# Optimization experiments

Measured on AMD Instinct MI355X. Metric: run time of the kernel, lower is better.

The kernel has to match this reference:

```python
import jax, jax.numpy as jnp
import numpy as np

D_MODEL = 1024
NUM_HEADS = 16
HEAD_DIM = D_MODEL // NUM_HEADS


def setup_inputs() -> dict:
    key = jax.random.key(0)
    ks = jax.random.split(key, 11)
    B, S = 4, 2048
    s = 1.0 / np.sqrt(D_MODEL)
    inp = {
        'query': jax.random.normal(ks[0], (B, S, D_MODEL), jnp.float32),
        'key': jax.random.normal(ks[1], (B, S, D_MODEL), jnp.float32),
        'value': jax.random.normal(ks[2], (B, S, D_MODEL), jnp.float32),
        'W_q': jax.random.normal(ks[3], (D_MODEL, D_MODEL), jnp.float32) * s,
        'b_q': jnp.zeros((D_MODEL,), jnp.float32),
        'W_k': jax.random.normal(ks[4], (D_MODEL, D_MODEL), jnp.float32) * s,
        'b_k': jnp.zeros((D_MODEL,), jnp.float32),
        'W_v': jax.random.normal(ks[5], (D_MODEL, D_MODEL), jnp.float32) * s,
        'b_v': jnp.zeros((D_MODEL,), jnp.float32),
        'W_o': jax.random.normal(ks[6], (D_MODEL, D_MODEL), jnp.float32) * s,
        'b_o': jnp.zeros((D_MODEL,), jnp.float32),
    }
    return inp


def reference(query, key, value, W_q, b_q, W_k, b_k, W_v, b_v, W_o, b_o):
    B, S, _ = query.shape
    # Linear projections (torch Linear: x @ W.T + b)
    Q = query @ W_q.T + b_q
    K = key @ W_k.T + b_k
    V = value @ W_v.T + b_v
    # [B, H, S, Dh]
    def split_heads(x):
        return x.reshape(B, -1, NUM_HEADS, HEAD_DIM).transpose(0, 2, 1, 3)
    Qh, Kh, Vh = split_heads(Q), split_heads(K), split_heads(V)
    scale = 1.0 / jnp.sqrt(jnp.float32(HEAD_DIM))
    scores = jnp.einsum('bhqd,bhkd->bhqk', Qh, Kh) * scale
    attn = jax.nn.softmax(scores, axis=-1)
    out = jnp.einsum('bhqk,bhkd->bhqd', attn, Vh)
    out = out.transpose(0, 2, 1, 3).reshape(B, S, D_MODEL)
    return out @ W_o.T + b_o
```

## Files before the change

kernel.cpp:

```cpp
#include <hip/hip_runtime.h>


#define BATCH 4
#define SEQ   2048
#define NH    16
#define DH    64
#define DM    1024
#define LOG2E 1.4426950408889634f
#define CSC   (0.125f * LOG2E)

typedef __attribute__((ext_vector_type(8))) short s16x8;
typedef __attribute__((ext_vector_type(4))) float f32x4;
typedef const __attribute__((address_space(1))) unsigned int* gas1;
typedef __attribute__((address_space(3))) unsigned int* las3;

__device__ __forceinline__ unsigned short f2bf(float f) {
  unsigned int u = __float_as_uint(f);
  u += 0x7FFFu + ((u >> 16) & 1u);
  return (unsigned short)(u >> 16);
}

__device__ __forceinline__ unsigned int cvt_pk_bf16(float lo, float hi) {
  unsigned int r;
  asm("v_cvt_pk_bf16_f32 %0, %1, %2" : "=v"(r) : "v"(lo), "v"(hi));
  return r;
}

__global__ __launch_bounds__(256) void cvt_bf16_k(const float* __restrict__ in,
                                                  unsigned short* __restrict__ out, int n4) {
  int i = blockIdx.x * 256 + threadIdx.x;
  if (i < n4) {
    float4 v = ((const float4*)in)[i];
    ushort4 o;
    o.x = f2bf(v.x); o.y = f2bf(v.y); o.z = f2bf(v.z); o.w = f2bf(v.w);
    ((ushort4*)out)[i] = o;
  }
}

template<bool BIAS_ROW, bool OUT_F32>
__global__ __launch_bounds__(256) void gemm_bt(const unsigned short* __restrict__ A,
                                               const unsigned short* __restrict__ Bm,
                                               const float* __restrict__ bias,
                                               void* __restrict__ Cout,
                                               int M, int N, int K) {
  __shared__ unsigned short As[128 * 64];
  __shared__ unsigned short Bs[128 * 64];
  const int tid = threadIdx.x;
  const int wave = tid >> 6, lane = tid & 63;
  const int lr = lane & 15, lh = lane >> 4;
  const int tM = blockIdx.y, tN = blockIdx.x;
  const int wm = (wave >> 1) * 64, wn = (wave & 1) * 64;
  f32x4 acc[4][4] = {};

  for (int k0 = 0; k0 < K; k0 += 64) {
    __syncthreads();
#pragma unroll
    for (int i = 0; i < 4; ++i) {
      const int slot = wave * 256 + i * 64 + lane;
      const int row = slot >> 3;
      const int cg = (slot & 7) ^ (row & 7);
      const unsigned short* ga = A  + (size_t)(tM * 128 + row) * K + k0 + cg * 8;
      const unsigned short* gb = Bm + (size_t)(tN * 128 + row) * K + k0 + cg * 8;
      __builtin_amdgcn_global_load_lds((gas1)ga, (las3)(As + (wave * 256 + i * 64) * 8), 16, 0, 0);
      __builtin_amdgcn_global_load_lds((gas1)gb, (las3)(Bs + (wave * 256 + i * 64) * 8), 16, 0, 0);
    }
    __syncthreads();

    s16x8 af[4][2], bfr[4][2];
#pragma unroll
    for (int mt = 0; mt < 4; ++mt) {
#pragma unroll
      for (int kt = 0; kt < 2; ++kt) {
        const int ra = wm + mt * 16 + lr;
        af[mt][kt] = *(const s16x8*)(As + ra * 64 + (((kt * 4 + lh) ^ (ra & 7)) * 8));
        const int rb = wn + mt * 16 + lr;
        bfr[mt][kt] = *(const s16x8*)(Bs + rb * 64 + (((kt * 4 + lh) ^ (rb & 7)) * 8));
      }
    }
#pragma unroll
    for (int mt = 0; mt < 4; ++mt) {
#pragma unroll
      for (int nt = 0; nt < 4; ++nt) {
        acc[mt][nt] = __builtin_amdgcn_mfma_f32_16x16x32_bf16(af[mt][0], bfr[nt][0], acc[mt][nt], 0, 0, 0);
        acc[mt][nt] = __builtin_amdgcn_mfma_f32_16x16x32_bf16(af[mt][1], bfr[nt][1], acc[mt][nt], 0, 0, 0);
      }
    }
  }

#pragma unroll
  for (int mt = 0; mt < 4; ++mt) {
#pragma unroll
    for (int nt = 0; nt < 4; ++nt) {
      const int row0 = tM * 128 + wm + mt * 16 + lh * 4;
      const int col  = tN * 128 + wn + nt * 16 + lr;
      const float bc = BIAS_ROW ? 0.f : bias[col];
#pragma unroll
      for (int r = 0; r < 4; ++r) {
        const float v = acc[mt][nt][r] + (BIAS_ROW ? bias[row0 + r] : bc);
        if (OUT_F32) ((float*)Cout)[(size_t)(row0 + r) * N + col] = v;
        else ((unsigned short*)Cout)[(size_t)(row0 + r) * N + col] = f2bf(v);
      }
    }
  }
}

__global__ __launch_bounds__(256) void attn_k(const unsigned short* __restrict__ Q,
                                              const unsigned short* __restrict__ Kp,
                                              const unsigned short* __restrict__ Vt,
                                              unsigned short* __restrict__ AO) {
  __shared__ unsigned short Ks[64 * 64];
  __shared__ unsigned short Vs[64 * 64];
  __shared__ unsigned short Ps[4 * 32 * 64];
  const int tid = threadIdx.x;
  const int w = tid >> 6, lane = tid & 63;
  const int lr = lane & 15, lh = lane >> 4;
  const int sw = lr & 7;

  const int id = blockIdx.x;
  const int g  = (id & 7) * 128 + (id >> 3);
  const int qt = g & 15;
  const int hb = g >> 4;
  const int h = hb & 15, b = hb >> 4;

  s16x8 qf[2][2];
#pragma unroll
  for (int qb = 0; qb < 2; ++qb)
#pragma unroll
    for (int kt = 0; kt < 2; ++kt)
      qf[qb][kt] = *(const s16x8*)(Q + (size_t)(b * SEQ + qt * 128 + w * 32 + qb * 16 + lr) * DM
                                     + h * DH + kt * 32 + lh * 8);

  f32x4 o[2][4] = {};
  float m_run[2] = {-1e30f, -1e30f};
  float l_run[2] = {0.f, 0.f};
  unsigned short* Pw = Ps + w * 2048;

  for (int kv0 = 0; kv0 < SEQ; kv0 += 64) {
    __syncthreads();
#pragma unroll
    for (int i = 0; i < 2; ++i) {
      const int slot = i * 256 + w * 64 + lane;
      const int row = slot >> 3;
      const int cg = (slot & 7) ^ (row & 7);
      const unsigned short* gk = Kp + (size_t)(b * SEQ + kv0 + row) * DM + h * DH + cg * 8;
      const unsigned short* gv = Vt + (size_t)(h * DH + row) * (BATCH * SEQ) + b * SEQ + kv0 + cg * 8;
      __builtin_amdgcn_global_load_lds((gas1)gk, (las3)(Ks + (i * 256 + w * 64) * 8), 16, 0, 0);
      __builtin_amdgcn_global_load_lds((gas1)gv, (las3)(Vs + (i * 256 + w * 64) * 8), 16, 0, 0);
    }
    __syncthreads();

    f32x4 s[2][4] = {};
#pragma unroll
    for (int nt = 0; nt < 4; ++nt) {
#pragma unroll
      for (int kt = 0; kt < 2; ++kt) {
        const s16x8 kf = *(const s16x8*)(Ks + (nt * 16 + lr) * 64 + (((kt * 4 + lh) ^ sw) * 8));
        s[0][nt] = __builtin_amdgcn_mfma_f32_16x16x32_bf16(kf, qf[0][kt], s[0][nt], 0, 0, 0);
        s[1][nt] = __builtin_amdgcn_mfma_f32_16x16x32_bf16(kf, qf[1][kt], s[1][nt], 0, 0, 0);
      }
    }

#pragma unroll
    for (int qb = 0; qb < 2; ++qb) {
      float mx = fmaxf(fmaxf(s[qb][0][0], s[qb][0][1]), fmaxf(s[qb][0][2], s[qb][0][3]));
#pragma unroll
      for (int nt = 1; nt < 4; ++nt)
        mx = fmaxf(mx, fmaxf(fmaxf(s[qb][nt][0], s[qb][nt][1]),
                             fmaxf(s[qb][nt][2], s[qb][nt][3])));
      mx = fmaxf(mx, __shfl_xor(mx, 16));
      mx = fmaxf(mx, __shfl_xor(mx, 32));
      if (!__all(mx - m_run[qb] <= 64.0f)) {
        const float al = __builtin_amdgcn_exp2f((m_run[qb] - mx) * CSC);
        m_run[qb] = mx;
        l_run[qb] *= al;
#pragma unroll
        for (int dt = 0; dt < 4; ++dt) o[qb][dt] *= al;
      }
      const float base = m_run[qb] * CSC;
      float p[4][4];
      float rs = 0.f;
#pragma unroll
      for (int nt = 0; nt < 4; ++nt)
#pragma unroll
        for (int r = 0; r < 4; ++r) {
          p[nt][r] = __builtin_amdgcn_exp2f(s[qb][nt][r] * CSC - base);
          rs += p[nt][r];
        }
      rs += __shfl_xor(rs, 16);
      rs += __shfl_xor(rs, 32);
      l_run[qb] += rs;

      const int qrow = qb * 16 + lr;
#pragma unroll
      for (int nt = 0; nt < 4; ++nt) {
        uint2 wd;
        wd.x = cvt_pk_bf16(p[nt][0], p[nt][1]);
        wd.y = cvt_pk_bf16(p[nt][2], p[nt][3]);
        const int c8 = nt * 2 + (lh >> 1);
        *(uint2*)(Pw + qrow * 64 + (((c8 ^ sw) << 3) | ((lh & 1) << 2))) = wd;
      }
    }

#pragma unroll
    for (int nb = 0; nb < 2; ++nb) {
      const s16x8 pf0 = *(const s16x8*)(Pw + lr * 64        + (((nb * 4 + lh) ^ sw) * 8));
      const s16x8 pf1 = *(const s16x8*)(Pw + (16 + lr) * 64 + (((nb * 4 + lh) ^ sw) * 8));
#pragma unroll
      for (int dt = 0; dt < 4; ++dt) {
        const s16x8 vf = *(const s16x8*)(Vs + (dt * 16 + lr) * 64 + (((nb * 4 + lh) ^ sw) * 8));
        o[0][dt] = __builtin_amdgcn_mfma_f32_16x16x32_bf16(vf, pf0, o[0][dt], 0, 0, 0);
        o[1][dt] = __builtin_amdgcn_mfma_f32_16x16x32_bf16(vf, pf1, o[1][dt], 0, 0, 0);
      }
    }
  }

#pragma unroll
  for (int qb = 0; qb < 2; ++qb) {
    const float rl = __builtin_amdgcn_rcpf(l_run[qb]);
    unsigned short* orow = AO + (size_t)(b * SEQ + qt * 128 + w * 32 + qb * 16 + lr) * DM + h * DH;
#pragma unroll
    for (int dt = 0; dt < 4; ++dt) {
      *(unsigned int*)(orow + dt * 16 + lh * 4)     = cvt_pk_bf16(o[qb][dt][0] * rl, o[qb][dt][1] * rl);
      *(unsigned int*)(orow + dt * 16 + lh * 4 + 2) = cvt_pk_bf16(o[qb][dt][2] * rl, o[qb][dt][3] * rl);
    }
  }
}

extern "C" void kernel_launch(void* const* d_in, const int* in_sizes, int n_in,
                              void* d_out, int out_size, void* d_ws, size_t ws_size,
                              hipStream_t stream) {
  const float* q   = (const float*)d_in[0];
  const float* k   = (const float*)d_in[1];
  const float* v   = (const float*)d_in[2];
  const float* W_q = (const float*)d_in[3];
  const float* b_q = (const float*)d_in[4];
  const float* W_k = (const float*)d_in[5];
  const float* b_k = (const float*)d_in[6];
  const float* W_v = (const float*)d_in[7];
  const float* b_v = (const float*)d_in[8];
  const float* W_o = (const float*)d_in[9];
  const float* b_o = (const float*)d_in[10];

  const size_t SD  = (size_t)BATCH * SEQ * DM;
  const size_t SDB = SD * 2;
  const size_t D2  = (size_t)DM * DM;
  if (ws_size < 5 * SDB + D2 * 2) return;

  char* base = (char*)d_ws;
  unsigned short* B0 = (unsigned short*)(base);
  unsigned short* B1 = (unsigned short*)(base + 1 * SDB);
  unsigned short* B2 = (unsigned short*)(base + 2 * SDB);
  unsigned short* B3 = (unsigned short*)(base + 3 * SDB);
  unsigned short* B4 = (unsigned short*)(base + 4 * SDB);
  unsigned short* Wb = (unsigned short*)(base + 5 * SDB);

  const int nSD4 = (int)(SD / 4), nD24 = (int)(D2 / 4);
  const dim3 blk(256);
  const dim3 gP(DM / 128, (BATCH * SEQ) / 128);
  const dim3 gV((BATCH * SEQ) / 128, DM / 128);
  const dim3 gA(16 * NH * BATCH);

  cvt_bf16_k<<<nSD4 / 256, blk, 0, stream>>>(q, B0, nSD4);
  cvt_bf16_k<<<nD24 / 256, blk, 0, stream>>>(W_q, Wb, nD24);
  gemm_bt<false, false><<<gP, blk, 0, stream>>>(B0, Wb, b_q, B3, BATCH * SEQ, DM, DM);
  cvt_bf16_k<<<nSD4 / 256, blk, 0, stream>>>(k, B1, nSD4);
  cvt_bf16_k<<<nD24 / 256, blk, 0, stream>>>(W_k, Wb, nD24);
  gemm_bt<false, false><<<gP, blk, 0, stream>>>(B1, Wb, b_k, B4, BATCH * SEQ, DM, DM);
  cvt_bf16_k<<<nSD4 / 256, blk, 0, stream>>>(v, B2, nSD4);
  cvt_bf16_k<<<nD24 / 256, blk, 0, stream>>>(W_v, Wb, nD24);
  gemm_bt<true, false><<<gV, blk, 0, stream>>>(Wb, B2, b_v, B1, DM, BATCH * SEQ, DM);
  attn_k<<<gA, blk, 0, stream>>>(B3, B4, B1, B0);
  cvt_bf16_k<<<nD24 / 256, blk, 0, stream>>>(W_o, Wb, nD24);
  gemm_bt<false, true><<<gP, blk, 0, stream>>>(B0, Wb, b_o, d_out, BATCH * SEQ, DM, DM);
}
```

Baseline: 255.0 us.

## Batch conversions and Q/K projections into fewer launches, double-buffer attention K/V

Merges the three activation conversions and the four weight conversions into two batched launches, and runs the Q and K projections together in one grid along z. Converted weights are staged in the output buffer until the final GEMM overwrites it. The attention kernel gains double-buffered K/V shared memory with explicit vmcnt waits, so the next tile loads while the current one computes. The goal is less launch overhead, better GPU fill, and hidden load latency, at the cost of twice the LDS use in attention, which may reduce occupancy.

Result: faster. 244.4 us (-4.1%).

```diff
diff --git a/kernel.cpp b/kernel.cpp
--- a/kernel.cpp
+++ b/kernel.cpp
@@ -26,29 +26,52 @@
   return r;
 }
 
-__global__ __launch_bounds__(256) void cvt_bf16_k(const float* __restrict__ in,
-                                                  unsigned short* __restrict__ out, int n4) {
+__global__ __launch_bounds__(256) void cvt3_k(const float* __restrict__ s0,
+                                              const float* __restrict__ s1,
+                                              const float* __restrict__ s2,
+                                              unsigned short* __restrict__ d0,
+                                              unsigned short* __restrict__ d1,
+                                              unsigned short* __restrict__ d2, int n4) {
+  const float* s = blockIdx.y == 0 ? s0 : blockIdx.y == 1 ? s1 : s2;
+  unsigned short* d = blockIdx.y == 0 ? d0 : blockIdx.y == 1 ? d1 : d2;
   int i = blockIdx.x * 256 + threadIdx.x;
   if (i < n4) {
-    float4 v = ((const float4*)in)[i];
+    float4 v = ((const float4*)s)[i];
     ushort4 o;
     o.x = f2bf(v.x); o.y = f2bf(v.y); o.z = f2bf(v.z); o.w = f2bf(v.w);
-    ((ushort4*)out)[i] = o;
+    ((ushort4*)d)[i] = o;
+  }
+}
+
+__global__ __launch_bounds__(256) void cvt4_k(const float* __restrict__ s0,
+                                              const float* __restrict__ s1,
+                                              const float* __restrict__ s2,
+                                              const float* __restrict__ s3,
+                                              unsigned short* __restrict__ d0,
+                                              unsigned short* __restrict__ d1,
+                                              unsigned short* __restrict__ d2,
+                                              unsigned short* __restrict__ d3, int n4) {
+  const float* s = blockIdx.y == 0 ? s0 : blockIdx.y == 1 ? s1 : blockIdx.y == 2 ? s2 : s3;
+  unsigned short* d = blockIdx.y == 0 ? d0 : blockIdx.y == 1 ? d1 : blockIdx.y == 2 ? d2 : d3;
+  int i = blockIdx.x * 256 + threadIdx.x;
+  if (i < n4) {
+    float4 v = ((const float4*)s)[i];
+    ushort4 o;
+    o.x = f2bf(v.x); o.y = f2bf(v.y); o.z = f2bf(v.z); o.w = f2bf(v.w);
+    ((ushort4*)d)[i] = o;
   }
 }
 
 template<bool BIAS_ROW, bool OUT_F32>
-__global__ __launch_bounds__(256) void gemm_bt(const unsigned short* __restrict__ A,
-                                               const unsigned short* __restrict__ Bm,
-                                               const float* __restrict__ bias,
-                                               void* __restrict__ Cout,
-                                               int M, int N, int K) {
-  __shared__ unsigned short As[128 * 64];
-  __shared__ unsigned short Bs[128 * 64];
+__device__ __forceinline__ void gemm_core(const unsigned short* __restrict__ A,
+                                          const unsigned short* __restrict__ Bm,
+                                          const float* __restrict__ bias,
+                                          void* __restrict__ Cout,
+                                          int M, int N, int K, int tM, int tN,
+                                          unsigned short* As, unsigned short* Bs) {
   const int tid = threadIdx.x;
   const int wave = tid >> 6, lane = tid & 63;
   const int lr = lane & 15, lh = lane >> 4;
-  const int tM = blockIdx.y, tN = blockIdx.x;
   const int wm = (wave >> 1) * 64, wn = (wave & 1) * 64;
   f32x4 acc[4][4] = {};
 
@@ -104,12 +127,38 @@
   }
 }
 
+template<bool BIAS_ROW, bool OUT_F32>
+__global__ __launch_bounds__(256) void gemm_bt(const unsigned short* __restrict__ A,
+                                               const unsigned short* __restrict__ Bm,
+                                               const float* __restrict__ bias,
+                                               void* __restrict__ Cout, int M, int N, int K) {
+  __shared__ unsigned short As[128 * 64];
+  __shared__ unsigned short Bs[128 * 64];
+  gemm_core<BIAS_ROW, OUT_F32>(A, Bm, bias, Cout, M, N, K, blockIdx.y, blockIdx.x, As, Bs);
+}
+
+__global__ __launch_bounds__(256) void gemm_qk(const unsigned short* __restrict__ A0,
+                                               const unsigned short* __restrict__ A1,
+                                               const unsigned short* __restrict__ W0,
+                                               const unsigned short* __restrict__ W1,
+                                               const float* __restrict__ c0,
+                                               const float* __restrict__ c1,
+                                               void* __restrict__ C0, void* __restrict__ C1,
+                                               int M, int N, int K) {
+  __shared__ unsigned short As[128 * 64];
+  __shared__ unsigned short Bs[128 * 64];
+  if (blockIdx.z == 0)
+    gemm_core<false, false>(A0, W0, c0, C0, M, N, K, blockIdx.y, blockIdx.x, As, Bs);
+  else
+    gemm_core<false, false>(A1, W1, c1, C1, M, N, K, blockIdx.y, blockIdx.x, As, Bs);
+}
+
 __global__ __launch_bounds__(256) void attn_k(const unsigned short* __restrict__ Q,
                                               const unsigned short* __restrict__ Kp,
                                               const unsigned short* __restrict__ Vt,
                                               unsigned short* __restrict__ AO) {
-  __shared__ unsigned short Ks[64 * 64];
-  __shared__ unsigned short Vs[64 * 64];
+  __shared__ unsigned short Ks[2][64 * 64];
+  __shared__ unsigned short Vs[2][64 * 64];
   __shared__ unsigned short Ps[4 * 32 * 64];
   const int tid = threadIdx.x;
   const int w = tid >> 6, lane = tid & 63;
@@ -129,32 +178,50 @@
     for (int kt = 0; kt < 2; ++kt)
       qf[qb][kt] = *(const s16x8*)(Q + (size_t)(b * SEQ + qt * 128 + w * 32 + qb * 16 + lr) * DM
                                      + h * DH + kt * 32 + lh * 8);
+  asm volatile("s_waitcnt vmcnt(0)" ::: "memory");
+  __builtin_amdgcn_sched_barrier(0);
 
   f32x4 o[2][4] = {};
   float m_run[2] = {-1e30f, -1e30f};
   float l_run[2] = {0.f, 0.f};
   unsigned short* Pw = Ps + w * 2048;
 
-  for (int kv0 = 0; kv0 < SEQ; kv0 += 64) {
-    __syncthreads();
+  const unsigned short* Kbase = Kp + (size_t)b * SEQ * DM + h * DH;
+  const unsigned short* Vbase = Vt + (size_t)h * DH * (BATCH * SEQ) + (size_t)b * SEQ;
+
+  auto stage = [&](int buf, int kv0) {
 #pragma unroll
     for (int i = 0; i < 2; ++i) {
       const int slot = i * 256 + w * 64 + lane;
       const int row = slot >> 3;
       const int cg = (slot & 7) ^ (row & 7);
-      const unsigned short* gk = Kp + (size_t)(b * SEQ + kv0 + row) * DM + h * DH + cg * 8;
-      const unsigned short* gv = Vt + (size_t)(h * DH + row) * (BATCH * SEQ) + b * SEQ + kv0 + cg * 8;
-      __builtin_amdgcn_global_load_lds((gas1)gk, (las3)(Ks + (i * 256 + w * 64) * 8), 16, 0, 0);
-      __builtin_amdgcn_global_load_lds((gas1)gv, (las3)(Vs + (i * 256 + w * 64) * 8), 16, 0, 0);
-    }
-    __syncthreads();
+      const unsigned short* gk = Kbase + (size_t)(kv0 + row) * DM + cg * 8;
+      const unsigned short* gv = Vbase + (size_t)row * (BATCH * SEQ) + kv0 + cg * 8;
+      __builtin_amdgcn_global_load_lds((gas1)gk, (las3)(&Ks[buf][(i * 256 + w * 64) * 8]), 16, 0, 0);
+      __builtin_amdgcn_global_load_lds((gas1)gv, (las3)(&Vs[buf][(i * 256 + w * 64) * 8]), 16, 0, 0);
+    }
+  };
+
+  stage(0, 0);
+  for (int t = 0; t < 32; ++t) {
+    const int cur = t & 1;
+    if (t < 31) {
+      stage(cur ^ 1, (t + 1) * 64);
+      asm volatile("s_waitcnt vmcnt(4)" ::: "memory");
+    } else {
+      asm volatile("s_waitcnt vmcnt(0)" ::: "memory");
+    }
+    __builtin_amdgcn_s_barrier();
+    __builtin_amdgcn_sched_barrier(0);
+    const unsigned short* Kc = Ks[cur];
+    const unsigned short* Vc = Vs[cur];
 
     f32x4 s[2][4] = {};
 #pragma unroll
     for (int nt = 0; nt < 4; ++nt) {
 #pragma unroll
       for (int kt = 0; kt < 2; ++kt) {
-        const s16x8 kf = *(const s16x8*)(Ks + (nt * 16 + lr) * 64 + (((kt * 4 + lh) ^ sw) * 8));
+        const s16x8 kf = *(const s16x8*)(Kc + (nt * 16 + lr) * 64 + (((kt * 4 + lh) ^ sw) * 8));
         s[0][nt] = __builtin_amdgcn_mfma_f32_16x16x32_bf16(kf, qf[0][kt], s[0][nt], 0, 0, 0);
         s[1][nt] = __builtin_amdgcn_mfma_f32_16x16x32_bf16(kf, qf[1][kt], s[1][nt], 0, 0, 0);
       }
@@ -207,11 +274,13 @@
       const s16x8 pf1 = *(const s16x8*)(Pw + (16 + lr) * 64 + (((nb * 4 + lh) ^ sw) * 8));
 #pragma unroll
       for (int dt = 0; dt < 4; ++dt) {
-        const s16x8 vf = *(const s16x8*)(Vs + (dt * 16 + lr) * 64 + (((nb * 4 + lh) ^ sw) * 8));
+        const s16x8 vf = *(const s16x8*)(Vc + (dt * 16 + lr) * 64 + (((nb * 4 + lh) ^ sw) * 8));
         o[0][dt] = __builtin_amdgcn_mfma_f32_16x16x32_bf16(vf, pf0, o[0][dt], 0, 0, 0);
         o[1][dt] = __builtin_amdgcn_mfma_f32_16x16x32_bf16(vf, pf1, o[1][dt], 0, 0, 0);
       }
     }
+    __builtin_amdgcn_sched_barrier(0);
+    __builtin_amdgcn_s_barrier();
   }
 
 #pragma unroll
@@ -254,22 +323,20 @@
   unsigned short* B4 = (unsigned short*)(base + 4 * SDB);
   unsigned short* Wb = (unsigned short*)(base + 5 * SDB);
 
+  unsigned short* dW0 = (unsigned short*)d_out;
+  unsigned short* dW1 = dW0 + D2;
+  unsigned short* dW2 = dW0 + 2 * D2;
+
   const int nSD4 = (int)(SD / 4), nD24 = (int)(D2 / 4);
   const dim3 blk(256);
-  const dim3 gP(DM / 128, (BATCH * SEQ) / 128);
-  const dim3 gV((BATCH * SEQ) / 128, DM / 128);
-  const dim3 gA(16 * NH * BATCH);
-
-  cvt_bf16_k<<<nSD4 / 256, blk, 0, stream>>>(q, B0, nSD4);
-  cvt_bf16_k<<<nD24 / 256, blk, 0, stream>>>(W_q, Wb, nD24);
-  gemm_bt<false, false><<<gP, blk, 0, stream>>>(B0, Wb, b_q, B3, BATCH * SEQ, DM, DM);
-  cvt_bf16_k<<<nSD4 / 256, blk, 0, stream>>>(k, B1, nSD4);
-  cvt_bf16_k<<<nD24 / 256, blk, 0, stream>>>(W_k, Wb, nD24);
-  gemm_bt<false, false><<<gP, blk, 0, stream>>>(B1, Wb, b_k, B4, BATCH * SEQ, DM, DM);
-  cvt_bf16_k<<<nSD4 / 256, blk, 0, stream>>>(v, B2, nSD4);
-  cvt_bf16_k<<<nD24 / 256, blk, 0, stream>>>(W_v, Wb, nD24);
-  gemm_bt<true, false><<<gV, blk, 0, stream>>>(Wb, B2, b_v, B1, DM, BATCH * SEQ, DM);
-  attn_k<<<gA, blk, 0, stream>>>(B3, B4, B1, B0);
-  cvt_bf16_k<<<nD24 / 256, blk, 0, stream>>>(W_o, Wb, nD24);
-  gemm_bt<false, true><<<gP, blk, 0, stream>>>(B0, Wb, b_o, d_out, BATCH * SEQ, DM, DM);
-}
+
+  cvt3_k<<<dim3(nSD4 / 256, 3), blk, 0, stream>>>(q, k, v, B0, B1, B2, nSD4);
+  cvt4_k<<<dim3(nD24 / 256, 4), blk, 0, stream>>>(W_q, W_k, W_v, W_o, dW0, dW1, dW2, Wb, nD24);
+  gemm_qk<<<dim3(DM / 128, (BATCH * SEQ) / 128, 2), blk, 0, stream>>>(
+      B0, B1, dW0, dW1, b_q, b_k, B3, B4, BATCH * SEQ, DM, DM);
+  gemm_bt<true, false><<<dim3((BATCH * SEQ) / 128, DM / 128), blk, 0, stream>>>(
+      dW2, B2, b_v, B1, DM, BATCH * SEQ, DM);
+  attn_k<<<dim3(16 * NH * BATCH), blk, 0, stream>>>(B3, B4, B1, B0);
+  gemm_bt<false, true><<<dim3(DM / 128, (BATCH * SEQ) / 128), blk, 0, stream>>>(
+      B0, Wb, b_o, d_out, BATCH * SEQ, DM, DM);
+}
```
